# Kernel tuning notes

Measured on AMD Instinct MI355X. Metric: run time of the kernel, lower is better.

## Reference

```python
import jax, jax.numpy as jnp
import numpy as np

B = 32768      # batch of head nodes
E = 1048576    # total edges (avg degree ~32)
DIM = 64
N_H, N_R, N_T = 3846, 60, 9366


def setup_inputs() -> dict:
    key = jax.random.key(0)
    k = jax.random.split(key, 7)
    h = jax.random.randint(k[0], (B,), 0, N_H)
    edge_seg = jnp.sort(jax.random.randint(k[1], (E,), 0, B))
    edge_rel = jax.random.randint(k[2], (E,), 0, N_R)
    edge_tail = jax.random.randint(k[3], (E,), 0, N_T)
    H_emb = jax.random.normal(k[4], (N_H, DIM), dtype=jnp.float32)
    R_emb = jax.random.normal(k[5], (N_R, DIM), dtype=jnp.float32)
    T_emb = jax.random.normal(k[6], (N_T, DIM), dtype=jnp.float32)
    return {"h": h, "edge_seg": edge_seg, "edge_rel": edge_rel,
            "edge_tail": edge_tail, "H_emb": H_emb, "R_emb": R_emb,
            "T_emb": T_emb}


def reference(h, edge_seg, edge_rel, edge_tail, H_emb, R_emb, T_emb):
    # Per-head embedding, gathered out to each of its edges.  [E, DIM]
    Hs = H_emb[h][edge_seg]
    R_v = R_emb[edge_rel]                  # [E, DIM]
    # Attention logits: dot(H_v[j], R_v[k]) per edge.  [E]
    scores = jnp.sum(Hs * R_v, axis=-1)
    # Segment (per-head) softmax over the ragged neighbor lists.
    m = jax.ops.segment_max(scores, edge_seg, num_segments=B)
    m = jnp.where(jnp.isfinite(m), m, jnp.float32(0.0))  # guard empty segs
    e = jnp.exp(scores - m[edge_seg])
    denom = jax.ops.segment_sum(e, edge_seg, num_segments=B)
    w = e / jnp.where(denom > 0, denom, jnp.float32(1.0))[edge_seg]
    # Original: Hv = (T_v - R_v) * score; V_New = sum over ALL elements
    # (a scalar), written into the whole row v_c[j].  Equivalently:
    contrib = w * jnp.sum(T_emb[edge_tail] - R_v, axis=-1)   # [E]
    vc_scalar = jax.ops.segment_sum(contrib, edge_seg, num_segments=B)  # [B]
    return jnp.broadcast_to(vc_scalar[:, None], (B, DIM))
```

## Files before the change

### kernel.cpp

```cpp
#include <hip/hip_runtime.h>
#include <math.h>


__global__ __launch_bounds__(256) void setup_k(
    const int* __restrict__ seg, int E, int B, int* __restrict__ seg_start,
    const float* __restrict__ H, const float* __restrict__ R,
    const float* __restrict__ T,
    float* __restrict__ S, float* __restrict__ tsum, float* __restrict__ rsum,
    int NH, int NR, int NT, int eBlocks, int sBlocks, int tBlocks)
{
    int b = blockIdx.x;

    if (b < eBlocks) {
        int e = b * 256 + threadIdx.x;
        if (e < E) {
            int cur = seg[e];
            if (e == 0) {
                for (int s = 0; s <= cur; ++s) seg_start[s] = 0;
            } else {
                int prev = seg[e - 1];
                for (int s = prev + 1; s <= cur; ++s) seg_start[s] = e;
            }
            if (e == E - 1) {
                for (int s = cur + 1; s <= B; ++s) seg_start[s] = E;
            }
        }
        return;
    }
    b -= eBlocks;

    if (b < sBlocks) {
        __shared__ float Rt[64 * 64];
        for (int t = threadIdx.x; t < NR * 64; t += 256) {
            int r = t >> 6, d = t & 63;
            Rt[d * NR + r] = R[t];
        }
        __syncthreads();

        int idx = b * 256 + threadIdx.x;
        if (idx < NH * NR) {
            int i = idx / NR;
            int r = idx - i * NR;
            const float4* h4 = (const float4*)(H + (size_t)i * 64);
            float acc = 0.f;
            #pragma unroll
            for (int q = 0; q < 16; ++q) {
                float4 hv = h4[q];
                int d = q * 4;
                acc = fmaf(hv.x, Rt[(d + 0) * NR + r], acc);
                acc = fmaf(hv.y, Rt[(d + 1) * NR + r], acc);
                acc = fmaf(hv.z, Rt[(d + 2) * NR + r], acc);
                acc = fmaf(hv.w, Rt[(d + 3) * NR + r], acc);
            }
            S[idx] = acc;
        }
        return;
    }
    b -= sBlocks;

    int lane = threadIdx.x & 63;
    if (b < tBlocks) {
        int row = b * 4 + (threadIdx.x >> 6);
        if (row < NT) {
            float v = T[(size_t)row * 64 + lane];
            #pragma unroll
            for (int off = 32; off; off >>= 1) v += __shfl_xor(v, off, 64);
            if (lane == 0) tsum[row] = v;
        }
        return;
    }
    b -= tBlocks;

    {
        int row = b * 4 + (threadIdx.x >> 6);
        if (row < NR) {
            float v = R[(size_t)row * 64 + lane];
            #pragma unroll
            for (int off = 32; off; off >>= 1) v += __shfl_xor(v, off, 64);
            if (lane == 0) rsum[row] = v;
        }
    }
}

__global__ __launch_bounds__(256) void main_k(
    const int* __restrict__ h,
    const int* __restrict__ edge_rel, const int* __restrict__ edge_tail,
    const float* __restrict__ S, const float* __restrict__ tsum,
    const float* __restrict__ rsum, const int* __restrict__ seg_start,
    float* __restrict__ out, int B, int NR)
{
    int grp = blockIdx.x * 8 + (threadIdx.x >> 5);
    int sub = threadIdx.x & 31;
    if (grp >= B) return;

    int lo = seg_start[grp];
    int hi = seg_start[grp + 1];
    int hh = h[grp];
    const float* Srow = S + (size_t)hh * NR;

    float m = -INFINITY, se = 0.f, sec = 0.f;
    for (int e = lo + sub; e < hi; e += 32) {
        int rel = edge_rel[e];
        int tl  = edge_tail[e];
        float sc = Srow[rel];
        float c  = tsum[tl] - rsum[rel];
        if (sc > m) {
            float f = __expf(m - sc);
            se *= f; sec *= f; m = sc;
        }
        float w = __expf(sc - m);
        se += w; sec = fmaf(w, c, sec);
    }

    #pragma unroll
    for (int off = 16; off; off >>= 1) {
        float m2   = __shfl_xor(m, off, 64);
        float se2  = __shfl_xor(se, off, 64);
        float sec2 = __shfl_xor(sec, off, 64);
        float M  = fmaxf(m, m2);
        float a  = (se  > 0.f) ? __expf(m  - M) : 0.f;
        float b2 = (se2 > 0.f) ? __expf(m2 - M) : 0.f;
        se  = se * a + se2 * b2;
        sec = sec * a + sec2 * b2;
        m = M;
    }

    float vc = (se > 0.f) ? (sec / se) : 0.f;
    float2 v2 = make_float2(vc, vc);
    *(float2*)(out + (size_t)grp * 64 + sub * 2) = v2;
}

extern "C" void kernel_launch(void* const* d_in, const int* in_sizes, int n_in,
                              void* d_out, int out_size, void* d_ws, size_t ws_size,
                              hipStream_t stream)
{
    const int*   h     = (const int*)d_in[0];
    const int*   eseg  = (const int*)d_in[1];
    const int*   erel  = (const int*)d_in[2];
    const int*   etail = (const int*)d_in[3];
    const float* Hv    = (const float*)d_in[4];
    const float* Rv    = (const float*)d_in[5];
    const float* Tv    = (const float*)d_in[6];

    int B  = in_sizes[0];
    int E  = in_sizes[1];
    int NH = in_sizes[4] / 64;
    int NR = in_sizes[5] / 64;
    int NT = in_sizes[6] / 64;

    char*  ws  = (char*)d_ws;
    size_t off = 0;
    auto alloc = [&](size_t bytes) -> void* {
        void* p = ws + off;
        off = (off + bytes + 255) & ~(size_t)255;
        return p;
    };
    int*   seg_start = (int*)  alloc((size_t)(B + 1) * sizeof(int));
    float* S         = (float*)alloc((size_t)NH * NR * sizeof(float));
    float* tsum      = (float*)alloc((size_t)NT * sizeof(float));
    float* rsum      = (float*)alloc((size_t)NR * sizeof(float));
    (void)ws_size;

    int eBlocks = (E + 255) / 256;
    int sBlocks = (NH * NR + 255) / 256;
    int tBlocks = (NT + 3) / 4;
    int rBlocks = (NR + 3) / 4;
    setup_k<<<eBlocks + sBlocks + tBlocks + rBlocks, 256, 0, stream>>>(
        eseg, E, B, seg_start, Hv, Rv, Tv, S, tsum, rsum,
        NH, NR, NT, eBlocks, sBlocks, tBlocks);

    main_k<<<(B + 7) / 8, 256, 0, stream>>>(
        h, erel, etail, S, tsum, rsum, seg_start, (float*)d_out, B, NR);
}
```

Before: 22.95 us.

## Drop online softmax max tracking by precomputing exp scores and exp*rsum table

The head-by-relation score table is replaced by a float2 table holding exp(score) and exp(score)*rsum. The main per-edge loop then needs only plain sums: no running max, no rescaling exponentials, and a simpler warp reduction. The tsum setup now uses float4 loads with 16 rows per block, rsum is computed in shared memory, and segment-start detection uses a wavefront shuffle. This gives up the max-subtraction safeguard, so large scores could overflow exp; it relies on the scores staying bounded.

```diff
diff --git a/kernel.cpp b/kernel.cpp
--- a/kernel.cpp
+++ b/kernel.cpp
@@ -6,24 +6,22 @@
     const int* __restrict__ seg, int E, int B, int* __restrict__ seg_start,
     const float* __restrict__ H, const float* __restrict__ R,
     const float* __restrict__ T,
-    float* __restrict__ S, float* __restrict__ tsum, float* __restrict__ rsum,
-    int NH, int NR, int NT, int eBlocks, int sBlocks, int tBlocks)
+    float2* __restrict__ P, float* __restrict__ tsum,
+    int NH, int NR, int NT, int eBlocks, int sBlocks)
 {
-    int b = blockIdx.x;
+    int b   = blockIdx.x;
+    int tid = threadIdx.x;
 
     if (b < eBlocks) {
-        int e = b * 256 + threadIdx.x;
+        int e = b * 256 + tid;
         if (e < E) {
-            int cur = seg[e];
-            if (e == 0) {
-                for (int s = 0; s <= cur; ++s) seg_start[s] = 0;
-            } else {
-                int prev = seg[e - 1];
-                for (int s = prev + 1; s <= cur; ++s) seg_start[s] = e;
-            }
-            if (e == E - 1) {
+            int lane = tid & 63;
+            int cur  = seg[e];
+            int prev = __shfl_up(cur, 1, 64);
+            if (lane == 0) prev = (e == 0) ? -1 : seg[e - 1];
+            for (int s = prev + 1; s <= cur; ++s) seg_start[s] = e;
+            if (e == E - 1)
                 for (int s = cur + 1; s <= B; ++s) seg_start[s] = E;
-            }
         }
         return;
     }
@@ -31,13 +29,21 @@
 
     if (b < sBlocks) {
         __shared__ float Rt[64 * 64];
-        for (int t = threadIdx.x; t < NR * 64; t += 256) {
+        __shared__ float rsum_s[64];
+        for (int t = tid; t < NR * 64; t += 256) {
             int r = t >> 6, d = t & 63;
             Rt[d * NR + r] = R[t];
         }
         __syncthreads();
+        if (tid < NR) {
+            float s = 0.f;
+            #pragma unroll 8
+            for (int d = 0; d < 64; ++d) s += Rt[d * NR + tid];
+            rsum_s[tid] = s;
+        }
+        __syncthreads();
 
-        int idx = b * 256 + threadIdx.x;
+        int idx = b * 256 + tid;
         if (idx < NH * NR) {
             int i = idx / NR;
             int r = idx - i * NR;
@@ -52,32 +58,24 @@
                 acc = fmaf(hv.z, Rt[(d + 2) * NR + r], acc);
                 acc = fmaf(hv.w, Rt[(d + 3) * NR + r], acc);
             }
-            S[idx] = acc;
+            float ex = __expf(acc);
+            P[idx] = make_float2(ex, ex * rsum_s[r]);
         }
         return;
     }
     b -= sBlocks;
 
-    int lane = threadIdx.x & 63;
-    if (b < tBlocks) {
-        int row = b * 4 + (threadIdx.x >> 6);
+    {
+        int lane = tid & 63;
+        int row  = b * 16 + (tid >> 6) * 4 + (lane >> 4);
         if (row < NT) {
-            float v = T[(size_t)row * 64 + lane];
-            #pragma unroll
-            for (int off = 32; off; off >>= 1) v += __shfl_xor(v, off, 64);
-            if (lane == 0) tsum[row] = v;
-        }
-        return;
-    }
-    b -= tBlocks;
-
-    {
-        int row = b * 4 + (threadIdx.x >> 6);
-        if (row < NR) {
-            float v = R[(size_t)row * 64 + lane];
-            #pragma unroll
-            for (int off = 32; off; off >>= 1) v += __shfl_xor(v, off, 64);
-            if (lane == 0) rsum[row] = v;
+            float4 v = ((const float4*)T)[(size_t)row * 16 + (lane & 15)];
+            float s = v.x + v.y + v.z + v.w;
+            s += __shfl_xor(s, 8, 64);
+            s += __shfl_xor(s, 4, 64);
+            s += __shfl_xor(s, 2, 64);
+            s += __shfl_xor(s, 1, 64);
+            if ((lane & 15) == 0) tsum[row] = s;
         }
     }
 }
@@ -85,8 +83,8 @@
 __global__ __launch_bounds__(256) void main_k(
     const int* __restrict__ h,
     const int* __restrict__ edge_rel, const int* __restrict__ edge_tail,
-    const float* __restrict__ S, const float* __restrict__ tsum,
-    const float* __restrict__ rsum, const int* __restrict__ seg_start,
+    const float2* __restrict__ P, const float* __restrict__ tsum,
+    const int* __restrict__ seg_start,
     float* __restrict__ out, int B, int NR)
 {
     int grp = blockIdx.x * 8 + (threadIdx.x >> 5);
@@ -95,39 +93,25 @@
 
     int lo = seg_start[grp];
     int hi = seg_start[grp + 1];
-    int hh = h[grp];
-    const float* Srow = S + (size_t)hh * NR;
+    const float2* Prow = P + (size_t)h[grp] * NR;
 
-    float m = -INFINITY, se = 0.f, sec = 0.f;
+    float se = 0.f, sec = 0.f;
     for (int e = lo + sub; e < hi; e += 32) {
         int rel = edge_rel[e];
         int tl  = edge_tail[e];
-        float sc = Srow[rel];
-        float c  = tsum[tl] - rsum[rel];
-        if (sc > m) {
-            float f = __expf(m - sc);
-            se *= f; sec *= f; m = sc;
-        }
-        float w = __expf(sc - m);
-        se += w; sec = fmaf(w, c, sec);
+        float2 pv = Prow[rel];
+        sec = fmaf(pv.x, tsum[tl], sec) - pv.y;
+        se += pv.x;
     }
 
     #pragma unroll
     for (int off = 16; off; off >>= 1) {
-        float m2   = __shfl_xor(m, off, 64);
-        float se2  = __shfl_xor(se, off, 64);
-        float sec2 = __shfl_xor(sec, off, 64);
-        float M  = fmaxf(m, m2);
-        float a  = (se  > 0.f) ? __expf(m  - M) : 0.f;
-        float b2 = (se2 > 0.f) ? __expf(m2 - M) : 0.f;
-        se  = se * a + se2 * b2;
-        sec = sec * a + sec2 * b2;
-        m = M;
+        se  += __shfl_xor(se, off, 64);
+        sec += __shfl_xor(sec, off, 64);
     }
 
     float vc = (se > 0.f) ? (sec / se) : 0.f;
-    float2 v2 = make_float2(vc, vc);
-    *(float2*)(out + (size_t)grp * 64 + sub * 2) = v2;
+    *(float2*)(out + (size_t)grp * 64 + sub * 2) = make_float2(vc, vc);
 }
 
 extern "C" void kernel_launch(void* const* d_in, const int* in_sizes, int n_in,
@@ -151,24 +135,22 @@
     char*  ws  = (char*)d_ws;
     size_t off = 0;
     auto alloc = [&](size_t bytes) -> void* {
-        void* p = ws + off;
+        void* q = ws + off;
         off = (off + bytes + 255) & ~(size_t)255;
-        return p;
+        return q;
     };
-    int*   seg_start = (int*)  alloc((size_t)(B + 1) * sizeof(int));
-    float* S         = (float*)alloc((size_t)NH * NR * sizeof(float));
-    float* tsum      = (float*)alloc((size_t)NT * sizeof(float));
-    float* rsum      = (float*)alloc((size_t)NR * sizeof(float));
+    float2* P         = (float2*)alloc((size_t)NH * NR * sizeof(float2));
+    float*  tsum      = (float*) alloc((size_t)NT * sizeof(float));
+    int*    seg_start = (int*)   alloc((size_t)(B + 1) * sizeof(int));
     (void)ws_size;
 
     int eBlocks = (E + 255) / 256;
     int sBlocks = (NH * NR + 255) / 256;
-    int tBlocks = (NT + 3) / 4;
-    int rBlocks = (NR + 3) / 4;
-    setup_k<<<eBlocks + sBlocks + tBlocks + rBlocks, 256, 0, stream>>>(
-        eseg, E, B, seg_start, Hv, Rv, Tv, S, tsum, rsum,
-        NH, NR, NT, eBlocks, sBlocks, tBlocks);
+    int tBlocks = (NT + 15) / 16;
+    setup_k<<<eBlocks + sBlocks + tBlocks, 256, 0, stream>>>(
+        eseg, E, B, seg_start, Hv, Rv, Tv, P, tsum, NH, NR, NT,
+        eBlocks, sBlocks);
 
     main_k<<<(B + 7) / 8, 256, 0, stream>>>(
-        h, erel, etail, S, tsum, rsum, seg_start, (float*)d_out, B, NR);
+        h, erel, etail, P, tsum, seg_start, (float*)d_out, B, NR);
 }
```

Result: slower. 25.05 us (+9.1%).
